# Optimization experiments

Measured on AMD Instinct MI355X. Metric: run time of the kernel, lower is better.

The kernel has to match this reference:

```python
import jax, jax.numpy as jnp
import numpy as np

B, TC, TQ, D = 32, 2048, 256, 256

def setup_inputs() -> dict:
    key = jax.random.key(0)
    k1, k2, k3 = jax.random.split(key, 3)
    context_emb = jax.random.normal(k1, (B, TC, D), dtype=jnp.float32)
    query_emb = jax.random.normal(k2, (B, TQ, D), dtype=jnp.float32)
    # nn.Linear(3d, 1, bias=False) weight flattened to [3d]
    w = jax.random.normal(k3, (3 * D,), dtype=jnp.float32) * (1.0 / np.sqrt(3 * D))
    return {"context_emb": context_emb, "query_emb": query_emb, "w": w}

def reference(context_emb, query_emb, w):
    d = context_emb.shape[-1]
    w1, w2, w3 = w[:d], w[d:2*d], w[2*d:]
    # Trilinear similarity S[b,t,q] = c.w1 + q.w2 + (c*q).w3 -- equivalent to
    # Linear over cat(c_ext, q_ext, c_ext*q_ext) without materializing [B,Tc,Tq,3d].
    S = (jnp.einsum('btd,d->bt', context_emb, w1)[:, :, None]
         + jnp.einsum('bqd,d->bq', query_emb, w2)[:, None, :]
         + jnp.einsum('btd,bqd->btq', context_emb * w3, query_emb))  # [B,Tc,Tq]
    S_softmax_row = jax.nn.softmax(S, axis=2)              # [B,Tc,Tq]
    b_t = jax.nn.softmax(jnp.max(S, axis=2), axis=1)       # [B,Tc]
    U_attention = jnp.einsum('btq,bqd->btd', S_softmax_row, query_emb)  # [B,Tc,d]
    h = jnp.einsum('bt,btd->bd', b_t, context_emb)         # [B,d]
    H_attention = h[:, None, :]                            # broadcast over Tc
    G = jnp.concatenate(
        (context_emb,
         U_attention,
         context_emb * U_attention,
         context_emb * H_attention), axis=-1)              # [B,Tc,4d]
    return G
```

## Files before the change

kernel.cpp:

```cpp
#include <hip/hip_runtime.h>

#define NB  32
#define NTC 2048
#define NTQ 256
#define ND  256

#define HP2_OFF 0
#define H_OFF   266240
#define Q2_OFF  274432
#define QBF_OFF 282624
#define QT_OFF  (282624 + 1048576)

#define PSTR 264

typedef __attribute__((ext_vector_type(8))) short short8v;
typedef __attribute__((ext_vector_type(4))) float float4v;
typedef unsigned int u32;

static __device__ inline short f2bf(float f) {
  union { float f; unsigned u; } v; v.f = f;
  unsigned r = v.u + 0x7FFFu + ((v.u >> 16) & 1u);
  return (short)(r >> 16);
}

static __device__ inline void gload_lds16(const short* g, short* l) {
  __builtin_amdgcn_global_load_lds(
      (const __attribute__((address_space(1))) u32*)g,
      (__attribute__((address_space(3))) u32*)l, 16, 0, 0);
}

__global__ __launch_bounds__(256) void k0_prep(const float* __restrict__ qry,
                                               const float* __restrict__ w,
                                               float* __restrict__ q2_ws,
                                               short* __restrict__ Qbf,
                                               short* __restrict__ Qt) {
  __shared__ float sRed[8][32];
  const int tid = threadIdx.x;
  const int b = blockIdx.x >> 3;
  const int q0 = (blockIdx.x & 7) << 5;
  const int q = tid & 31;
  const int dc = tid >> 5;
  const float* src = qry + (((size_t)b * NTQ) + q0 + q) * ND + dc * 32;
  const float* w2p = w + ND + dc * 32;

  float vals[32];
  float part = 0.f;
  #pragma unroll
  for (int i = 0; i < 8; ++i) {
    float4 v = *(const float4*)(src + 4 * i);
    float4 u = *(const float4*)(w2p + 4 * i);
    part += v.x*u.x + v.y*u.y + v.z*u.z + v.w*u.w;
    vals[4*i] = v.x; vals[4*i+1] = v.y; vals[4*i+2] = v.z; vals[4*i+3] = v.w;
  }
  short pk[32];
  #pragma unroll
  for (int i = 0; i < 32; ++i) pk[i] = f2bf(vals[i]);

  short* dst = Qbf + ((size_t)b * NTQ + q0 + q) * ND + dc * 32;
  #pragma unroll
  for (int i = 0; i < 4; ++i) *(short8v*)(dst + 8 * i) = *(short8v*)(pk + 8 * i);
  short* dstT = Qt + (size_t)b * NTQ * ND + q0 + q;
  #pragma unroll
  for (int i = 0; i < 32; ++i) dstT[(size_t)(dc * 32 + i) * NTQ] = pk[i];

  part += __shfl_xor(part, 32);
  if ((tid & 32) == 0) sRed[dc][q] = part;
  __syncthreads();
  if (tid < 32) {
    float s = sRed[0][tid] + sRed[2][tid] + sRed[4][tid] + sRed[6][tid];
    q2_ws[b * NTQ + q0 + tid] = s;
  }
}

__global__ __launch_bounds__(256, 2) void k1_main(const float* __restrict__ ctx,
                                                  const float* __restrict__ w,
                                                  const short* __restrict__ Qbf,
                                                  const short* __restrict__ Qt,
                                                  const float* __restrict__ q2_ws,
                                                  float* __restrict__ hp2,
                                                  float* __restrict__ G) {
  __shared__ __align__(16) short sStage[2][256 * 32];
  __shared__ __align__(16) short sP_all[4 * 16 * PSTR];
  __shared__ __align__(16) float sW[768];
  __shared__ __align__(16) float sHall[4][256];
  __shared__ float sRedM[4], sRedZ[4];

  const int tid  = threadIdx.x;
  const int wv   = tid >> 6;
  const int lane = tid & 63;
  const int g    = lane >> 4;
  const int li   = lane & 15;
  const int bid  = blockIdx.x;
  const int obid = (bid & 7) * 128 + (bid >> 3);
  const int b    = obid >> 5;
  const int tile = obid & 31;
  const int t0   = tile << 6;

  short* sPw = sP_all + wv * (16 * PSTR);

  const float* __restrict__ ctxB = ctx + ((size_t)b * NTC + t0) * ND;
  const short* __restrict__ Qb   = Qbf + (size_t)b * NTQ * ND;
  const short* __restrict__ Qtb  = Qt  + (size_t)b * NTQ * ND;

  const int srow = 64 * wv + (lane >> 2);
  const int sblk = lane & 3;

  #define STAGE(buf, src, c0)                                                   \
    { _Pragma("unroll")                                                         \
      for (int j = 0; j < 4; ++j) {                                             \
        const int row_ = srow + 16 * j;                                         \
        const int gi_  = sblk ^ ((row_ >> 1) & 3);                              \
        gload_lds16((src) + (size_t)row_ * 256 + (c0) + 8 * gi_,                \
                    &sStage[buf][wv * 2048 + j * 512]);                         \
      } }

  #define STAGE2(buf, cc)                                                       \
    { _Pragma("unroll")                                                         \
      for (int j = 0; j < 4; ++j) {                                             \
        const int slot_ = (wv * 4 + j) * 64 + lane;                             \
        const int row_  = slot_ >> 5;                                           \
        const int gr_   = slot_ & 31;                                           \
        gload_lds16(Qtb + (size_t)(32 * (cc) + row_) * 256 + 8 * (gr_ ^ (row_ & 7)), \
                    &sStage[buf][wv * 2048 + j * 512]);                         \
      } }

  float4v acc[16];
  #pragma unroll
  for (int n = 0; n < 16; ++n) acc[n] = (float4v)0.f;
  float s1part = 0.f;

  float q2v[16];
  #pragma unroll
  for (int n = 0; n < 16; ++n) q2v[n] = q2_ws[b * NTQ + 16 * n + li];
  if (tid < 192) *(float4*)(sW + 4 * tid) = *(const float4*)(w + 4 * tid);
  STAGE(0, Qb, 0);
  const float* arow = ctxB + (size_t)(16 * wv + li) * ND + 8 * g;
  float4 Ac0 = *(const float4*)(arow);
  float4 Ac1 = *(const float4*)(arow + 4);
  asm volatile("s_waitcnt vmcnt(0) lgkmcnt(0)" ::: "memory");
  __builtin_amdgcn_s_barrier();
  __builtin_amdgcn_sched_barrier(0);

  const size_t gb0 = ((size_t)b * NTC + t0 + 16 * wv + li) * 1024 + 8 * g;

  #pragma unroll
  for (int c = 0; c < 8; ++c) {
    float4 u0 = *(const float4*)(sW + 32 * c + 8 * g);
    float4 u1 = *(const float4*)(sW + 32 * c + 8 * g + 4);
    float4 v0 = *(const float4*)(sW + 512 + 32 * c + 8 * g);
    float4 v1 = *(const float4*)(sW + 512 + 32 * c + 8 * g + 4);
    s1part += Ac0.x*u0.x + Ac0.y*u0.y + Ac0.z*u0.z + Ac0.w*u0.w
            + Ac1.x*u1.x + Ac1.y*u1.y + Ac1.z*u1.z + Ac1.w*u1.w;
    short8v af;
    af[0]=f2bf(Ac0.x*v0.x); af[1]=f2bf(Ac0.y*v0.y); af[2]=f2bf(Ac0.z*v0.z); af[3]=f2bf(Ac0.w*v0.w);
    af[4]=f2bf(Ac1.x*v1.x); af[5]=f2bf(Ac1.y*v1.y); af[6]=f2bf(Ac1.z*v1.z); af[7]=f2bf(Ac1.w*v1.w);
    __builtin_amdgcn_sched_barrier(0);
    float4 An0, An1;
    if (c < 7) {
      An0 = *(const float4*)(arow + 32 * (c + 1));
      An1 = *(const float4*)(arow + 32 * (c + 1) + 4);
    }
    __builtin_amdgcn_sched_barrier(0);
    if (c < 7) { STAGE((c + 1) & 1, Qb, 32 * (c + 1)); }
    else       { STAGE2(0, 0); }
    __builtin_amdgcn_sched_barrier(0);
    asm volatile("s_waitcnt vmcnt(6)" ::: "memory");
    __builtin_amdgcn_s_barrier();
    __builtin_amdgcn_sched_barrier(0);
    const short* sb = sStage[c & 1];
    #pragma unroll
    for (int n = 0; n < 16; ++n) {
      const int row = 16 * n + li;
      short8v bb = *(const short8v*)(sb + row * 32 + 8 * (g ^ ((row >> 1) & 3)));
      acc[n] = __builtin_amdgcn_mfma_f32_16x16x32_bf16(af, bb, acc[n], 0, 0, 0);
    }
    *(float4*)(G + gb0 + 32 * c)     = Ac0;
    *(float4*)(G + gb0 + 32 * c + 4) = Ac1;
    __builtin_amdgcn_sched_barrier(0);
    __builtin_amdgcn_s_barrier();
    __builtin_amdgcn_sched_barrier(0);
    Ac0 = An0; Ac1 = An1;
  }

  s1part += __shfl_xor(s1part, 16);
  s1part += __shfl_xor(s1part, 32);
  float s1r[4];
  #pragma unroll
  for (int r = 0; r < 4; ++r) s1r[r] = __shfl(s1part, 4 * g + r);

  #pragma unroll
  for (int n = 0; n < 16; ++n)
    #pragma unroll
    for (int r = 0; r < 4; ++r) acc[n][r] += s1r[r] + q2v[n];

  float mx[4], inv[4];
  #pragma unroll
  for (int r = 0; r < 4; ++r) {
    float m0 = acc[0][r];
    #pragma unroll
    for (int n = 1; n < 16; ++n) m0 = fmaxf(m0, acc[n][r]);
    m0 = fmaxf(m0, __shfl_xor(m0, 1));
    m0 = fmaxf(m0, __shfl_xor(m0, 2));
    m0 = fmaxf(m0, __shfl_xor(m0, 4));
    m0 = fmaxf(m0, __shfl_xor(m0, 8));
    mx[r] = m0;
  }
  #pragma unroll
  for (int r = 0; r < 4; ++r) {
    float z = 0.f;
    #pragma unroll
    for (int n = 0; n < 16; ++n) { float e = __expf(acc[n][r] - mx[r]); acc[n][r] = e; z += e; }
    z += __shfl_xor(z, 1);
    z += __shfl_xor(z, 2);
    z += __shfl_xor(z, 4);
    z += __shfl_xor(z, 8);
    inv[r] = 1.0f / z;
  }
  #pragma unroll
  for (int n = 0; n < 16; ++n) {
    #pragma unroll
    for (int r = 0; r < 4; ++r)
      sPw[(4 * g + r) * PSTR + 16 * n + li] = f2bf(acc[n][r] * inv[r]);
  }

  float lm = fmaxf(fmaxf(mx[0], mx[1]), fmaxf(mx[2], mx[3]));
  lm = fmaxf(lm, __shfl_xor(lm, 16));
  lm = fmaxf(lm, __shfl_xor(lm, 32));
  if (lane == 0) sRedM[wv] = lm;
  __builtin_amdgcn_sched_barrier(0);
  asm volatile("s_waitcnt lgkmcnt(0)" ::: "memory");
  __builtin_amdgcn_s_barrier();
  __builtin_amdgcn_sched_barrier(0);
  const float Mloc = fmaxf(fmaxf(sRedM[0], sRedM[1]), fmaxf(sRedM[2], sRedM[3]));
  float wgt[4];
  float zp = 0.f;
  #pragma unroll
  for (int r = 0; r < 4; ++r) { wgt[r] = __expf(mx[r] - Mloc); zp += wgt[r]; }
  zp += __shfl_xor(zp, 16);
  zp += __shfl_xor(zp, 32);
  if (lane == 0) sRedZ[wv] = zp;

  #pragma unroll
  for (int cc = 0; cc < 8; ++cc) {
    if (cc < 7) { STAGE2((cc + 1) & 1, cc + 1); }
    __builtin_amdgcn_sched_barrier(0);
    if (cc < 7) asm volatile("s_waitcnt vmcnt(4)" ::: "memory");
    else        asm volatile("s_waitcnt vmcnt(0)" ::: "memory");
    __builtin_amdgcn_s_barrier();
    __builtin_amdgcn_sched_barrier(0);
    const short* sb = sStage[cc & 1];
    float4v uacc0 = (float4v)0.f, uacc1 = (float4v)0.f;
    #pragma unroll
    for (int ks = 0; ks < 8; ++ks) {
      short8v a2 = *(const short8v*)(sPw + li * PSTR + 32 * ks + 8 * g);
      short8v b0 = *(const short8v*)(sb + (li)      * 256 + 8 * ((4 * ks + g) ^ (li & 7)));
      short8v b1 = *(const short8v*)(sb + (16 + li) * 256 + 8 * ((4 * ks + g) ^ (li & 7)));
      uacc0 = __builtin_amdgcn_mfma_f32_16x16x32_bf16(a2, b0, uacc0, 0, 0, 0);
      uacc1 = __builtin_amdgcn_mfma_f32_16x16x32_bf16(a2, b1, uacc1, 0, 0, 0);
    }
    __builtin_amdgcn_sched_barrier(0);
    __builtin_amdgcn_s_barrier();
    __builtin_amdgcn_sched_barrier(0);
    float hc0 = 0.f, hc1 = 0.f;
    #pragma unroll
    for (int r = 0; r < 4; ++r) {
      const int trow = 16 * wv + 4 * g + r;
      const size_t gb = ((size_t)b * NTC + t0 + trow) * 1024 + 32 * cc;
      const float* cp = ctxB + (size_t)trow * ND + 32 * cc;
      const float c0 = cp[li];
      const float c1 = cp[16 + li];
      const float uu0 = uacc0[r];
      const float uu1 = uacc1[r];
      G[gb + 256 + li]      = uu0;
      G[gb + 256 + 16 + li] = uu1;
      G[gb + 512 + li]      = c0 * uu0;
      G[gb + 512 + 16 + li] = c1 * uu1;
      hc0 += wgt[r] * c0;
      hc1 += wgt[r] * c1;
    }
    hc0 += __shfl_xor(hc0, 16); hc0 += __shfl_xor(hc0, 32);
    hc1 += __shfl_xor(hc1, 16); hc1 += __shfl_xor(hc1, 32);
    if (g == 0) {
      sHall[wv][32 * cc + li]      = hc0;
      sHall[wv][32 * cc + 16 + li] = hc1;
    }
  }

  __syncthreads();
  float* hp = hp2 + (size_t)(b * 32 + tile) * 260;
  {
    const int d = tid & 255;
    float ph = sHall[0][d] + sHall[1][d] + sHall[2][d] + sHall[3][d];
    hp[d] = ph;
  }
  if (tid == 0) {
    hp[256] = Mloc;
    hp[257] = sRedZ[0] + sRedZ[1] + sRedZ[2] + sRedZ[3];
  }
  #undef STAGE
  #undef STAGE2
}

__global__ __launch_bounds__(256) void k2h(const float* __restrict__ hp2,
                                           float* __restrict__ h_ws) {
  __shared__ float sM2[32], sZ2[32];
  const int b = blockIdx.x;
  const int tid = threadIdx.x;
  if (tid < 32) {
    sM2[tid] = hp2[(size_t)(b * 32 + tid) * 260 + 256];
    sZ2[tid] = hp2[(size_t)(b * 32 + tid) * 260 + 257];
  }
  __syncthreads();
  float M = -1e30f;
  #pragma unroll
  for (int i = 0; i < 32; ++i) M = fmaxf(M, sM2[i]);
  float Z = 0.f;
  float a = 0.f;
  #pragma unroll
  for (int i = 0; i < 32; ++i) {
    float e = __expf(sM2[i] - M);
    Z += sZ2[i] * e;
    a += hp2[(size_t)(b * 32 + i) * 260 + tid] * e;
  }
  h_ws[b * 256 + tid] = a / Z;
}

__global__ __launch_bounds__(256) void k3_epi(const float* __restrict__ ctx,
                                              const float* __restrict__ h_ws,
                                              float* __restrict__ G) {
  size_t f = (size_t)blockIdx.x * 256 + threadIdx.x;
  size_t e = f * 4;
  int d = (int)(e & 255);
  size_t bt = e >> 8;
  int b = (int)(bt >> 11);
  float4 c = *(const float4*)(ctx + e);
  float4 h = *(const float4*)(h_ws + b * ND + d);
  *(float4*)(G + bt * 1024 + 768 + d) =
      make_float4(c.x * h.x, c.y * h.y, c.z * h.z, c.w * h.w);
}

extern "C" void kernel_launch(void* const* d_in, const int* in_sizes, int n_in,
                              void* d_out, int out_size, void* d_ws, size_t ws_size,
                              hipStream_t stream) {
  const float* ctx = (const float*)d_in[0];
  const float* qry = (const float*)d_in[1];
  const float* w   = (const float*)d_in[2];
  float* G  = (float*)d_out;
  float* ws = (float*)d_ws;
  float* hp2   = ws + HP2_OFF;
  float* h_ws  = ws + H_OFF;
  float* q2_ws = ws + Q2_OFF;
  short* Qbf = (short*)(ws + QBF_OFF);
  short* Qt  = (short*)(ws + QT_OFF);

  k0_prep<<<NB * 8, 256, 0, stream>>>(qry, w, q2_ws, Qbf, Qt);
  k1_main<<<NB * (NTC / 64), 256, 0, stream>>>(ctx, w, Qbf, Qt, q2_ws, hp2, G);
  k2h<<<NB, 256, 0, stream>>>(hp2, h_ws);
  k3_epi<<<16384, 256, 0, stream>>>(ctx, h_ws, G);
}
```

Measured before the change: 103.5 us.

## Transpose score MFMA and keep softmax probabilities in registers via shuffles

```diff
diff --git a/kernel.cpp b/kernel.cpp
--- a/kernel.cpp
+++ b/kernel.cpp
@@ -10,8 +10,6 @@
 #define Q2_OFF  274432
 #define QBF_OFF 282624
 #define QT_OFF  (282624 + 1048576)
-
-#define PSTR 264
 
 typedef __attribute__((ext_vector_type(8))) short short8v;
 typedef __attribute__((ext_vector_type(4))) float float4v;
@@ -72,7 +70,7 @@
   }
 }
 
-__global__ __launch_bounds__(256, 2) void k1_main(const float* __restrict__ ctx,
+__global__ __launch_bounds__(256, 4) void k1_main(const float* __restrict__ ctx,
                                                   const float* __restrict__ w,
                                                   const short* __restrict__ Qbf,
                                                   const short* __restrict__ Qt,
@@ -80,8 +78,8 @@
                                                   float* __restrict__ hp2,
                                                   float* __restrict__ G) {
   __shared__ __align__(16) short sStage[2][256 * 32];
-  __shared__ __align__(16) short sP_all[4 * 16 * PSTR];
-  __shared__ __align__(16) float sW[768];
+  __shared__ __align__(16) float sW[512];
+  __shared__ __align__(16) float sQ2[256];
   __shared__ __align__(16) float sHall[4][256];
   __shared__ float sRedM[4], sRedZ[4];
 
@@ -96,8 +94,6 @@
   const int tile = obid & 31;
   const int t0   = tile << 6;
 
-  short* sPw = sP_all + wv * (16 * PSTR);
-
   const float* __restrict__ ctxB = ctx + ((size_t)b * NTC + t0) * ND;
   const short* __restrict__ Qb   = Qbf + (size_t)b * NTQ * ND;
   const short* __restrict__ Qtb  = Qt  + (size_t)b * NTQ * ND;
@@ -129,10 +125,9 @@
   for (int n = 0; n < 16; ++n) acc[n] = (float4v)0.f;
   float s1part = 0.f;
 
-  float q2v[16];
-  #pragma unroll
-  for (int n = 0; n < 16; ++n) q2v[n] = q2_ws[b * NTQ + 16 * n + li];
-  if (tid < 192) *(float4*)(sW + 4 * tid) = *(const float4*)(w + 4 * tid);
+  if (tid < 64)       *(float4*)(sW + 4 * tid) = *(const float4*)(w + 4 * tid);
+  else if (tid < 128) *(float4*)(sW + 4 * tid) = *(const float4*)(w + 512 + 4 * tid - 256);
+  else if (tid < 192) *(float4*)(sQ2 + 4 * (tid - 128)) = *(const float4*)(q2_ws + b * NTQ + 4 * (tid - 128));
   STAGE(0, Qb, 0);
   const float* arow = ctxB + (size_t)(16 * wv + li) * ND + 8 * g;
   float4 Ac0 = *(const float4*)(arow);
@@ -147,8 +142,8 @@
   for (int c = 0; c < 8; ++c) {
     float4 u0 = *(const float4*)(sW + 32 * c + 8 * g);
     float4 u1 = *(const float4*)(sW + 32 * c + 8 * g + 4);
-    float4 v0 = *(const float4*)(sW + 512 + 32 * c + 8 * g);
-    float4 v1 = *(const float4*)(sW + 512 + 32 * c + 8 * g + 4);
+    float4 v0 = *(const float4*)(sW + 256 + 32 * c + 8 * g);
+    float4 v1 = *(const float4*)(sW + 256 + 32 * c + 8 * g + 4);
     s1part += Ac0.x*u0.x + Ac0.y*u0.y + Ac0.z*u0.z + Ac0.w*u0.w
             + Ac1.x*u1.x + Ac1.y*u1.y + Ac1.z*u1.z + Ac1.w*u1.w;
     short8v af;
@@ -164,7 +159,8 @@
     if (c < 7) { STAGE((c + 1) & 1, Qb, 32 * (c + 1)); }
     else       { STAGE2(0, 0); }
     __builtin_amdgcn_sched_barrier(0);
-    asm volatile("s_waitcnt vmcnt(6)" ::: "memory");
+    if (c == 7) asm volatile("s_waitcnt vmcnt(6)" ::: "memory");
+    else        asm volatile("s_waitcnt vmcnt(8)" ::: "memory");
     __builtin_amdgcn_s_barrier();
     __builtin_amdgcn_sched_barrier(0);
     const short* sb = sStage[c & 1];
@@ -172,7 +168,7 @@
     for (int n = 0; n < 16; ++n) {
       const int row = 16 * n + li;
       short8v bb = *(const short8v*)(sb + row * 32 + 8 * (g ^ ((row >> 1) & 3)));
-      acc[n] = __builtin_amdgcn_mfma_f32_16x16x32_bf16(af, bb, acc[n], 0, 0, 0);
+      acc[n] = __builtin_amdgcn_mfma_f32_16x16x32_bf16(bb, af, acc[n], 0, 0, 0);
     }
     *(float4*)(G + gb0 + 32 * c)     = Ac0;
     *(float4*)(G + gb0 + 32 * c + 4) = Ac1;
@@ -184,79 +180,99 @@
 
   s1part += __shfl_xor(s1part, 16);
   s1part += __shfl_xor(s1part, 32);
-  float s1r[4];
-  #pragma unroll
-  for (int r = 0; r < 4; ++r) s1r[r] = __shfl(s1part, 4 * g + r);
-
+  #pragma unroll
+  for (int n = 0; n < 16; ++n) {
+    float4 qv = *(const float4*)(sQ2 + 16 * n + 4 * g);
+    acc[n][0] += s1part + qv.x;
+    acc[n][1] += s1part + qv.y;
+    acc[n][2] += s1part + qv.z;
+    acc[n][3] += s1part + qv.w;
+  }
+  float mx = acc[0][0];
   #pragma unroll
   for (int n = 0; n < 16; ++n)
     #pragma unroll
-    for (int r = 0; r < 4; ++r) acc[n][r] += s1r[r] + q2v[n];
-
-  float mx[4], inv[4];
-  #pragma unroll
-  for (int r = 0; r < 4; ++r) {
-    float m0 = acc[0][r];
-    #pragma unroll
-    for (int n = 1; n < 16; ++n) m0 = fmaxf(m0, acc[n][r]);
-    m0 = fmaxf(m0, __shfl_xor(m0, 1));
-    m0 = fmaxf(m0, __shfl_xor(m0, 2));
-    m0 = fmaxf(m0, __shfl_xor(m0, 4));
-    m0 = fmaxf(m0, __shfl_xor(m0, 8));
-    mx[r] = m0;
-  }
-  #pragma unroll
-  for (int r = 0; r < 4; ++r) {
-    float z = 0.f;
-    #pragma unroll
-    for (int n = 0; n < 16; ++n) { float e = __expf(acc[n][r] - mx[r]); acc[n][r] = e; z += e; }
-    z += __shfl_xor(z, 1);
-    z += __shfl_xor(z, 2);
-    z += __shfl_xor(z, 4);
-    z += __shfl_xor(z, 8);
-    inv[r] = 1.0f / z;
-  }
-  #pragma unroll
-  for (int n = 0; n < 16; ++n) {
-    #pragma unroll
-    for (int r = 0; r < 4; ++r)
-      sPw[(4 * g + r) * PSTR + 16 * n + li] = f2bf(acc[n][r] * inv[r]);
-  }
-
-  float lm = fmaxf(fmaxf(mx[0], mx[1]), fmaxf(mx[2], mx[3]));
-  lm = fmaxf(lm, __shfl_xor(lm, 16));
-  lm = fmaxf(lm, __shfl_xor(lm, 32));
-  if (lane == 0) sRedM[wv] = lm;
+    for (int r = 0; r < 4; ++r) mx = fmaxf(mx, acc[n][r]);
+  mx = fmaxf(mx, __shfl_xor(mx, 16));
+  mx = fmaxf(mx, __shfl_xor(mx, 32));
+  float z = 0.f;
+  #pragma unroll
+  for (int n = 0; n < 16; ++n)
+    #pragma unroll
+    for (int r = 0; r < 4; ++r) { float e = __expf(acc[n][r] - mx); acc[n][r] = e; z += e; }
+  z += __shfl_xor(z, 16);
+  z += __shfl_xor(z, 32);
+  const float inv = 1.0f / z;
+
+  float tm = mx;
+  tm = fmaxf(tm, __shfl_xor(tm, 1));
+  tm = fmaxf(tm, __shfl_xor(tm, 2));
+  tm = fmaxf(tm, __shfl_xor(tm, 4));
+  tm = fmaxf(tm, __shfl_xor(tm, 8));
+  if (lane == 0) sRedM[wv] = tm;
   __builtin_amdgcn_sched_barrier(0);
   asm volatile("s_waitcnt lgkmcnt(0)" ::: "memory");
   __builtin_amdgcn_s_barrier();
   __builtin_amdgcn_sched_barrier(0);
   const float Mloc = fmaxf(fmaxf(sRedM[0], sRedM[1]), fmaxf(sRedM[2], sRedM[3]));
-  float wgt[4];
-  float zp = 0.f;
-  #pragma unroll
-  for (int r = 0; r < 4; ++r) { wgt[r] = __expf(mx[r] - Mloc); zp += wgt[r]; }
-  zp += __shfl_xor(zp, 16);
-  zp += __shfl_xor(zp, 32);
+  const float wgt = __expf(mx - Mloc);
+  float zp = wgt;
+  zp += __shfl_xor(zp, 1);
+  zp += __shfl_xor(zp, 2);
+  zp += __shfl_xor(zp, 4);
+  zp += __shfl_xor(zp, 8);
   if (lane == 0) sRedZ[wv] = zp;
+  float wgtRow[4];
+  #pragma unroll
+  for (int r = 0; r < 4; ++r) wgtRow[r] = __shfl(wgt, 4 * g + r);
+
+  int pkx[16], pky[16];
+  #pragma unroll
+  for (int n = 0; n < 16; ++n) {
+    pkx[n] = (int)(u32)(unsigned short)f2bf(acc[n][0] * inv)
+           | ((int)(u32)(unsigned short)f2bf(acc[n][1] * inv) << 16);
+    pky[n] = (int)(u32)(unsigned short)f2bf(acc[n][2] * inv)
+           | ((int)(u32)(unsigned short)f2bf(acc[n][3] * inv) << 16);
+  }
+  const int srcLow  = ((g & 1) << 5) + li;
+  const int srcHigh = srcLow + 16;
+  const bool hiSel  = (g >= 2);
+  short8v a2f[8];
+  #pragma unroll
+  for (int ks = 0; ks < 8; ++ks) {
+    int eL0 = __shfl(pkx[2 * ks],     srcLow);
+    int eL1 = __shfl(pky[2 * ks],     srcLow);
+    int oL0 = __shfl(pkx[2 * ks + 1], srcLow);
+    int oL1 = __shfl(pky[2 * ks + 1], srcLow);
+    int eH0 = __shfl(pkx[2 * ks],     srcHigh);
+    int eH1 = __shfl(pky[2 * ks],     srcHigh);
+    int oH0 = __shfl(pkx[2 * ks + 1], srcHigh);
+    int oH1 = __shfl(pky[2 * ks + 1], srcHigh);
+    union { int i[4]; short8v s; } u;
+    u.i[0] = hiSel ? oL0 : eL0;
+    u.i[1] = hiSel ? oL1 : eL1;
+    u.i[2] = hiSel ? oH0 : eH0;
+    u.i[3] = hiSel ? oH1 : eH1;
+    a2f[ks] = u.s;
+  }
 
   #pragma unroll
   for (int cc = 0; cc < 8; ++cc) {
     if (cc < 7) { STAGE2((cc + 1) & 1, cc + 1); }
     __builtin_amdgcn_sched_barrier(0);
-    if (cc < 7) asm volatile("s_waitcnt vmcnt(4)" ::: "memory");
-    else        asm volatile("s_waitcnt vmcnt(0)" ::: "memory");
+    if (cc == 0)      asm volatile("s_waitcnt vmcnt(6)"  ::: "memory");
+    else if (cc == 7) asm volatile("s_waitcnt vmcnt(24)" ::: "memory");
+    else              asm volatile("s_waitcnt vmcnt(28)" ::: "memory");
     __builtin_amdgcn_s_barrier();
     __builtin_amdgcn_sched_barrier(0);
     const short* sb = sStage[cc & 1];
     float4v uacc0 = (float4v)0.f, uacc1 = (float4v)0.f;
     #pragma unroll
     for (int ks = 0; ks < 8; ++ks) {
-      short8v a2 = *(const short8v*)(sPw + li * PSTR + 32 * ks + 8 * g);
       short8v b0 = *(const short8v*)(sb + (li)      * 256 + 8 * ((4 * ks + g) ^ (li & 7)));
       short8v b1 = *(const short8v*)(sb + (16 + li) * 256 + 8 * ((4 * ks + g) ^ (li & 7)));
-      uacc0 = __builtin_amdgcn_mfma_f32_16x16x32_bf16(a2, b0, uacc0, 0, 0, 0);
-      uacc1 = __builtin_amdgcn_mfma_f32_16x16x32_bf16(a2, b1, uacc1, 0, 0, 0);
+      uacc0 = __builtin_amdgcn_mfma_f32_16x16x32_bf16(a2f[ks], b0, uacc0, 0, 0, 0);
+      uacc1 = __builtin_amdgcn_mfma_f32_16x16x32_bf16(a2f[ks], b1, uacc1, 0, 0, 0);
     }
     __builtin_amdgcn_sched_barrier(0);
     __builtin_amdgcn_s_barrier();
@@ -275,8 +291,8 @@
       G[gb + 256 + 16 + li] = uu1;
       G[gb + 512 + li]      = c0 * uu0;
       G[gb + 512 + 16 + li] = c1 * uu1;
-      hc0 += wgt[r] * c0;
-      hc1 += wgt[r] * c1;
+      hc0 += wgtRow[r] * c0;
+      hc1 += wgtRow[r] * c1;
     }
     hc0 += __shfl_xor(hc0, 16); hc0 += __shfl_xor(hc0, 32);
     hc1 += __shfl_xor(hc1, 16); hc1 += __shfl_xor(hc1, 32);
```

Result: faster. 94.42 us (-8.8%).
